# Performance work log

Hardware: AMD Instinct MI355X
Metric: run time of the kernel (lower is better)

## Reference

```python
import jax, jax.numpy as jnp
import numpy as np
from jax import lax

# dims
B, H, W, C = 32, 64, 64, 256
FEATURES, HEADS, NQ = 256, 8, 2
K, STRIDE, PAD = 3, 2, 1
HD = FEATURES // HEADS  # head dim = 32


def setup_inputs() -> dict:
    key = jax.random.key(0)
    ks = jax.random.split(key, 7)
    x = jax.random.normal(ks[0], (B, H, W, C), jnp.float32)
    # learned shared queries: truncated normal * sqrt(1/head_dim)
    query = jax.random.truncated_normal(ks[1], -2.0, 2.0, (NQ, FEATURES), jnp.float32) * np.float32(np.sqrt(1.0 / HD))
    Wk = jax.random.normal(ks[2], (C, FEATURES), jnp.float32) * np.float32(np.sqrt(1.0 / C))  # lecun
    Wv = jax.random.normal(ks[3], (C, FEATURES), jnp.float32) * np.float32(np.sqrt(1.0 / C))
    rpe_bias = jax.random.truncated_normal(ks[4], -2.0, 2.0, (K * K, NQ * HEADS), jnp.float32) * np.float32(0.02)
    attn_scale_w = jax.random.normal(ks[5], (K * K, NQ * HEADS), jnp.float32) * np.float32(0.02)
    Wo = jax.random.normal(ks[6], (FEATURES, FEATURES), jnp.float32) * np.float32(np.sqrt(1.0 / FEATURES))
    return {"x": x, "query": query, "Wk": Wk, "Wv": Wv,
            "rpe_bias": rpe_bias, "attn_scale_w": attn_scale_w, "Wo": Wo}


def _qna_forward(x, query, Wk, Wv, rpe_bias, attn_scale_w, Wo):
    # --- queries: reshape to [NQ, HEADS, HD], unit-normalize per head, depth-scale ---
    q = query.reshape(NQ, HEADS, HD)
    q = q / (jnp.linalg.norm(q, axis=-1, keepdims=True) + 1e-6)
    q = q / jnp.sqrt(HD).astype(q.dtype)

    # --- fused QK: (q Wk^T) applied to x, never materializing per-window keys ---
    Wk_r = Wk.reshape(C, HEADS, HD)
    qWk = jnp.einsum('qHd,DHd->DqH', q, Wk_r)              # [C, NQ, HEADS]
    cost = jnp.einsum('bijD,DqH->bijqH', x, qWk)            # [B, H, W, NQ, HEADS]
    cost_exp = jnp.exp(cost - lax.stop_gradient(jnp.max(cost)))  # global shift, cancels in softmax

    # --- values ---
    v = jnp.einsum('bijD,DF->bijF', x, Wv)                  # [B, H, W, FEATURES]
    v_cost_exp = cost_exp[..., None] * v.reshape(B, H, W, 1, HEADS, HD)
    v_cost_exp = v_cost_exp.reshape(B, H, W, NQ * FEATURES)

    # --- relative position bias + per-offset query mixing scale ---
    rpe = rpe_bias.reshape(K, K, 1, NQ * HEADS)
    rpe_exp = jnp.exp(rpe - lax.stop_gradient(jnp.max(rpe)))  # shift cancels (appears in num & den)
    scale = attn_scale_w.reshape(K, K, 1, NQ * HEADS)
    num_kernel = jnp.repeat(rpe_exp * scale, HD, axis=-1)   # [K, K, 1, NQ*FEATURES]

    # numerator: windowed sum of exp(cost)*v weighted by exp(rpe)*scale (depthwise conv)
    num = lax.conv_general_dilated(
        v_cost_exp, num_kernel, window_strides=(STRIDE, STRIDE),
        padding=((PAD, PAD), (PAD, PAD)), feature_group_count=NQ * FEATURES,
        dimension_numbers=('NHWC', 'HWIO', 'NHWC'))
    # denominator: windowed sum of exp(cost) weighted by exp(rpe)
    den = lax.conv_general_dilated(
        cost_exp.reshape(B, H, W, NQ * HEADS), rpe_exp, window_strides=(STRIDE, STRIDE),
        padding=((PAD, PAD), (PAD, PAD)), feature_group_count=NQ * HEADS,
        dimension_numbers=('NHWC', 'HWIO', 'NHWC'))
    ho, wo = num.shape[1], num.shape[2]

    out = num.reshape(B, ho, wo, NQ, HEADS, HD) / den.reshape(B, ho, wo, NQ, HEADS, 1)
    out = out.sum(axis=3).reshape(B, ho, wo, FEATURES)      # combine queries
    return jnp.einsum('bijF,FO->bijO', out, Wo)             # output projection


def reference(x, query, Wk, Wv, rpe_bias, attn_scale_w, Wo):
    return _qna_forward(x, query, Wk, Wv, rpe_bias, attn_scale_w, Wo)
```

## Files before the change

kernel.cpp:

```cpp
#include <hip/hip_runtime.h>
#include <math.h>

typedef __attribute__((ext_vector_type(8))) short bf16x8;
typedef __attribute__((ext_vector_type(4))) float floatx4;

static __device__ __forceinline__ short f2bf(float f) {
    union { float f; unsigned u; } a; a.f = f;
    unsigned r = a.u + 0x7fffu + ((a.u >> 16) & 1u);
    return (short)(r >> 16);
}
static __device__ __forceinline__ float bf2f(short s) {
    union { unsigned u; float f; } c; c.u = ((unsigned)(unsigned short)s) << 16;
    return c.f;
}

__global__ __launch_bounds__(256) void prep_kernel(
    const float* __restrict__ query,
    const float* __restrict__ Wk,
    const float* __restrict__ rpe_bias,
    const float* __restrict__ attn_scale_w,
    const float* __restrict__ Wv,
    const float* __restrict__ Wo,
    float* __restrict__ rpe_exp,
    float* __restrict__ rpe_scale,
    short* __restrict__ Bq,
    short* __restrict__ Wvh,
    short* __restrict__ Bo)
{
    __shared__ float qn[16 * 33];
    __shared__ float Wt[16][260];
    __shared__ float qwk_s[16][17];
    int tid = threadIdx.x, bb = blockIdx.x;

    for (int i = tid; i < 512; i += 256) {
        int qq  = i >> 8;
        int rem = i & 255;
        int h   = rem >> 5;
        int d   = rem & 31;
        qn[((qq << 3) + h) * 33 + d] = query[i];
    }
    for (int i = tid; i < 16 * 256; i += 256)
        Wt[i >> 8][i & 255] = Wk[bb * 16 * 256 + i];
    __syncthreads();
    if (tid < 16) {
        float s = 0.f;
        #pragma unroll
        for (int d = 0; d < 32; ++d) { float t = qn[tid * 33 + d]; s += t * t; }
        float inv = 1.0f / ((sqrtf(s) + 1e-6f) * sqrtf(32.0f));
        #pragma unroll
        for (int d = 0; d < 32; ++d) qn[tid * 33 + d] *= inv;
    }
    __syncthreads();

    int g  = tid & 15;
    int Dl = tid >> 4;
    int h2 = g & 7;
    float acc = 0.f;
    #pragma unroll
    for (int d = 0; d < 32; ++d)
        acc += qn[g * 33 + d] * Wt[Dl][h2 * 32 + d];
    qwk_s[Dl][g] = acc;
    __syncthreads();

    {
        int kl = tid >> 4, gg = tid & 15;
        int k  = bb * 16 + kl;
        int kc = k >> 5, q5 = k & 31, qd = q5 >> 3, j = q5 & 7;
        int lane = qd * 16 + gg;
        Bq[kc * 512 + lane * 8 + j] = f2bf(qwk_s[kl][gg]);
    }

    for (int kl = 0; kl < 16; ++kl) {
        int k  = bb * 16 + kl;
        int kc = k >> 5, q5 = k & 31, qd = q5 >> 3, j = q5 & 7;
        int n  = tid;
        int gg = n & 15;
        int lane = qd * 16 + gg;
        float vv = Wv[k * 256 + n];
        float vo = Wo[k * 256 + n];
        int nt  = n >> 4;
        Wvh[nt * 4096 + kc * 512 + lane * 8 + j] = f2bf(vv);
        Bo[nt * 4096 + kc * 512 + lane * 8 + j]  = f2bf(vo);
    }

    if (bb == 0 && tid < 144) {
        float r = expf(rpe_bias[tid]);
        rpe_exp[tid]   = r;
        rpe_scale[tid] = r * attn_scale_w[tid];
    }
}

#define XROWA 264
__global__ __launch_bounds__(256) void va_kernel(
    const float* __restrict__ x,
    const short* __restrict__ Bq,
    const short* __restrict__ Wvh,
    short* __restrict__ V,
    float* __restrict__ cesg)
{
    __shared__ short XA[64 * XROWA];
    int tid  = threadIdx.x;
    int lane = tid & 63, wv = tid >> 6;
    int m16  = lane & 15, quad = lane >> 4;
    size_t p0 = (size_t)blockIdx.x * 64;

    #pragma unroll
    for (int i = 0; i < 8; ++i) {
        int it  = tid + i * 256;
        int row = it >> 5, l = it & 31;
        const float* xp = x + (p0 + row) * 256 + l * 8;
        float4 f0 = *(const float4*)xp;
        float4 f1 = *(const float4*)(xp + 4);
        bf16x8 s;
        s[0] = f2bf(f0.x); s[1] = f2bf(f0.y); s[2] = f2bf(f0.z); s[3] = f2bf(f0.w);
        s[4] = f2bf(f1.x); s[5] = f2bf(f1.y); s[6] = f2bf(f1.z); s[7] = f2bf(f1.w);
        *(bf16x8*)&XA[row * XROWA + l * 8] = s;
    }
    __syncthreads();

    bf16x8 Arow[8];
    const short* xrow = &XA[(wv * 16 + m16) * XROWA + quad * 8];
    #pragma unroll
    for (int kc = 0; kc < 8; ++kc)
        Arow[kc] = *(const bf16x8*)(xrow + kc * 32);
    __syncthreads();

    {
        floatx4 acc = (floatx4){0.f, 0.f, 0.f, 0.f};
        const short* bq = Bq + lane * 8;
        #pragma unroll
        for (int kc = 0; kc < 8; ++kc)
            acc = __builtin_amdgcn_mfma_f32_16x16x32_bf16(
                      Arow[kc], *(const bf16x8*)(bq + kc * 512), acc, 0, 0, 0);
        #pragma unroll
        for (int r = 0; r < 4; ++r)
            cesg[(p0 + wv * 16 + quad * 4 + r) * 16 + m16] = expf(acc[r]);
    }

    #pragma unroll 4
    for (int nt = 0; nt < 16; ++nt) {
        floatx4 acc = (floatx4){0.f, 0.f, 0.f, 0.f};
        const short* bp = Wvh + nt * 4096 + lane * 8;
        #pragma unroll
        for (int kc = 0; kc < 8; ++kc)
            acc = __builtin_amdgcn_mfma_f32_16x16x32_bf16(
                      Arow[kc], *(const bf16x8*)(bp + kc * 512), acc, 0, 0, 0);
        #pragma unroll
        for (int r = 0; r < 4; ++r)
            XA[(wv * 16 + quad * 4 + r) * XROWA + nt * 16 + m16] = f2bf(acc[r]);
    }
    __syncthreads();

    #pragma unroll
    for (int i = 0; i < 8; ++i) {
        int it  = tid + i * 256;
        int row = it >> 5, l = it & 31;
        *(bf16x8*)&V[(p0 + row) * 256 + l * 8] =
            *(const bf16x8*)&XA[row * XROWA + l * 8];
    }
}

#define OROW 264
__global__ __launch_bounds__(512) void qb_kernel(
    const float* __restrict__ cesg,
    const short* __restrict__ V,
    const float* __restrict__ rpe_exp,
    const float* __restrict__ rpe_scale,
    const short* __restrict__ Bo,
    float* __restrict__ out)
{
    __shared__ short out_tr[16 * OROW];
    __shared__ float wcoefs[8][9][16];
    __shared__ float invden[16][16];

    int tid  = threadIdx.x;
    int lane = tid & 63, wv = tid >> 6;
    int m16  = lane & 15, quad = lane >> 4;

    int blk0 = blockIdx.x;
    int blk  = ((blk0 & 7) << 8) | (blk0 >> 3);
    int b   = blk >> 6;
    int io  = (blk >> 1) & 31;
    int hf  = blk & 1;
    int i0  = io * 2 - 1;
    int jbase = hf * 32 - 1;

    if (tid < 256) {
        int op = tid >> 4, g = tid & 15;
        float den = 0.f;
        #pragma unroll
        for (int w = 0; w < 9; ++w) {
            int ky = w / 3, kx = w - ky * 3;
            int ii = i0 + ky, jj = jbase + 2 * op + kx;
            if ((unsigned)ii < 64u && (unsigned)jj < 64u) {
                size_t pix = ((size_t)((b << 6) + ii) << 6) + jj;
                den = fmaf(rpe_exp[w * 16 + g], cesg[pix * 16 + g], den);
            }
        }
        invden[op][g] = 1.0f / den;
    }
    __syncthreads();

    for (int it = tid; it < 1152; it += 512) {
        int op = it / 72, r = it - op * 72;
        int w = r >> 3, h = r & 7;
        int ky = w / 3, kx = w - ky * 3;
        int ii = i0 + ky, jj = jbase + 2 * op + kx;
        float v = 0.f;
        if ((unsigned)ii < 64u && (unsigned)jj < 64u) {
            size_t pix = ((size_t)((b << 6) + ii) << 6) + jj;
            v = cesg[pix * 16 + h]     * rpe_scale[w * 16 + h]     * invden[op][h] +
                cesg[pix * 16 + 8 + h] * rpe_scale[w * 16 + 8 + h] * invden[op][8 + h];
        }
        wcoefs[h][w][op] = v;
    }
    __syncthreads();

    {
        int op = tid >> 5;
        int nc = tid & 31;
        int h  = nc >> 2;
        float wcv[9];
        #pragma unroll
        for (int w = 0; w < 9; ++w) wcv[w] = wcoefs[h][w][op];

        float o[8];
        #pragma unroll
        for (int j = 0; j < 8; ++j) o[j] = 0.f;
        #pragma unroll
        for (int w = 0; w < 9; ++w) {
            int ky = w / 3, kx = w - ky * 3;
            int ii = i0 + ky, jj = jbase + 2 * op + kx;
            bool valid = ((unsigned)ii < 64u) && ((unsigned)jj < 64u);
            size_t pix = valid ? (((size_t)((b << 6) + ii) << 6) + jj) : 0;
            bf16x8 vv = *(const bf16x8*)&V[pix * 256 + nc * 8];
            #pragma unroll
            for (int j = 0; j < 8; ++j)
                o[j] = fmaf(wcv[w], bf2f(vv[j]), o[j]);
        }
        bf16x8 ob;
        #pragma unroll
        for (int j = 0; j < 8; ++j) ob[j] = f2bf(o[j]);
        *(bf16x8*)&out_tr[op * OROW + nc * 8] = ob;
    }
    __syncthreads();

    {
        floatx4 acc0 = (floatx4){0.f, 0.f, 0.f, 0.f};
        floatx4 acc1 = (floatx4){0.f, 0.f, 0.f, 0.f};
        int nt0 = wv * 2;
        const short* bp = Bo + nt0 * 4096 + lane * 8;
        #pragma unroll
        for (int kc = 0; kc < 8; ++kc) {
            bf16x8 a  = *(const bf16x8*)&out_tr[m16 * OROW + kc * 32 + quad * 8];
            bf16x8 b0 = *(const bf16x8*)(bp + kc * 512);
            bf16x8 b1 = *(const bf16x8*)(bp + 4096 + kc * 512);
            acc0 = __builtin_amdgcn_mfma_f32_16x16x32_bf16(a, b0, acc0, 0, 0, 0);
            acc1 = __builtin_amdgcn_mfma_f32_16x16x32_bf16(a, b1, acc1, 0, 0, 0);
        }
        size_t op0 = (size_t)blk * 16;
        #pragma unroll
        for (int r = 0; r < 4; ++r) {
            out[(op0 + quad * 4 + r) * 256 + nt0 * 16 + m16]       = acc0[r];
            out[(op0 + quad * 4 + r) * 256 + (nt0 + 1) * 16 + m16] = acc1[r];
        }
    }
}

extern "C" void kernel_launch(void* const* d_in, const int* in_sizes, int n_in,
                              void* d_out, int out_size, void* d_ws, size_t ws_size,
                              hipStream_t stream)
{
    const float* x     = (const float*)d_in[0];
    const float* query = (const float*)d_in[1];
    const float* Wk    = (const float*)d_in[2];
    const float* Wv    = (const float*)d_in[3];
    const float* rpe   = (const float*)d_in[4];
    const float* asw   = (const float*)d_in[5];
    const float* Wo    = (const float*)d_in[6];
    float* out = (float*)d_out;

    float* ws        = (float*)d_ws;
    float* rpe_exp   = ws;
    float* rpe_scale = ws + 144;
    short* Bq        = (short*)(ws + 288);
    short* Wvh       = (short*)(ws + 288 + 2048);
    short* Bo        = (short*)(ws + 288 + 2048 + 32768);
    short* V         = (short*)(ws + 68608);
    float* cesg      = ws + 68608 + 16777216;

    prep_kernel<<<dim3(16), dim3(256), 0, stream>>>(query, Wk, rpe, asw, Wv, Wo,
                                                    rpe_exp, rpe_scale, Bq, Wvh, Bo);
    va_kernel<<<dim3(2048), dim3(256), 0, stream>>>(x, Bq, Wvh, V, cesg);
    qb_kernel<<<dim3(2048), dim3(512), 0, stream>>>(cesg, V, rpe_exp, rpe_scale,
                                                    Bo, out);
}
```

Measured before the change: 289.2 us.

## Retile V projection so each wave owns an N-slice across all rows

```diff
diff --git a/kernel.cpp b/kernel.cpp
--- a/kernel.cpp
+++ b/kernel.cpp
@@ -91,7 +91,7 @@
 }
 
 #define XROWA 264
-__global__ __launch_bounds__(256) void va_kernel(
+__global__ __launch_bounds__(256, 4) void va_kernel(
     const float* __restrict__ x,
     const short* __restrict__ Bq,
     const short* __restrict__ Wvh,
@@ -118,37 +118,54 @@
     }
     __syncthreads();
 
-    bf16x8 Arow[8];
-    const short* xrow = &XA[(wv * 16 + m16) * XROWA + quad * 8];
-    #pragma unroll
-    for (int kc = 0; kc < 8; ++kc)
-        Arow[kc] = *(const bf16x8*)(xrow + kc * 32);
-    __syncthreads();
-
     {
         floatx4 acc = (floatx4){0.f, 0.f, 0.f, 0.f};
-        const short* bq = Bq + lane * 8;
-        #pragma unroll
-        for (int kc = 0; kc < 8; ++kc)
+        const short* bq   = Bq + lane * 8;
+        const short* xrow = &XA[(wv * 16 + m16) * XROWA + quad * 8];
+        #pragma unroll
+        for (int kc = 0; kc < 8; ++kc) {
+            bf16x8 a = *(const bf16x8*)(xrow + kc * 32);
             acc = __builtin_amdgcn_mfma_f32_16x16x32_bf16(
-                      Arow[kc], *(const bf16x8*)(bq + kc * 512), acc, 0, 0, 0);
+                      a, *(const bf16x8*)(bq + kc * 512), acc, 0, 0, 0);
+        }
         #pragma unroll
         for (int r = 0; r < 4; ++r)
             cesg[(p0 + wv * 16 + quad * 4 + r) * 16 + m16] = expf(acc[r]);
     }
 
-    #pragma unroll 4
-    for (int nt = 0; nt < 16; ++nt) {
-        floatx4 acc = (floatx4){0.f, 0.f, 0.f, 0.f};
-        const short* bp = Wvh + nt * 4096 + lane * 8;
-        #pragma unroll
-        for (int kc = 0; kc < 8; ++kc)
-            acc = __builtin_amdgcn_mfma_f32_16x16x32_bf16(
-                      Arow[kc], *(const bf16x8*)(bp + kc * 512), acc, 0, 0, 0);
-        #pragma unroll
-        for (int r = 0; r < 4; ++r)
-            XA[(wv * 16 + quad * 4 + r) * XROWA + nt * 16 + m16] = f2bf(acc[r]);
-    }
+    floatx4 acc[4][4];
+    #pragma unroll
+    for (int m = 0; m < 4; ++m)
+        #pragma unroll
+        for (int ln = 0; ln < 4; ++ln)
+            acc[m][ln] = (floatx4){0.f, 0.f, 0.f, 0.f};
+
+    const short* bvw = Wvh + (4 * wv) * 4096 + lane * 8;
+    #pragma unroll
+    for (int kc = 0; kc < 8; ++kc) {
+        bf16x8 B0 = *(const bf16x8*)(bvw + 0 * 4096 + kc * 512);
+        bf16x8 B1 = *(const bf16x8*)(bvw + 1 * 4096 + kc * 512);
+        bf16x8 B2 = *(const bf16x8*)(bvw + 2 * 4096 + kc * 512);
+        bf16x8 B3 = *(const bf16x8*)(bvw + 3 * 4096 + kc * 512);
+        #pragma unroll
+        for (int m = 0; m < 4; ++m) {
+            bf16x8 a = *(const bf16x8*)&XA[(m * 16 + m16) * XROWA + kc * 32 + quad * 8];
+            acc[m][0] = __builtin_amdgcn_mfma_f32_16x16x32_bf16(a, B0, acc[m][0], 0, 0, 0);
+            acc[m][1] = __builtin_amdgcn_mfma_f32_16x16x32_bf16(a, B1, acc[m][1], 0, 0, 0);
+            acc[m][2] = __builtin_amdgcn_mfma_f32_16x16x32_bf16(a, B2, acc[m][2], 0, 0, 0);
+            acc[m][3] = __builtin_amdgcn_mfma_f32_16x16x32_bf16(a, B3, acc[m][3], 0, 0, 0);
+        }
+    }
+    __syncthreads();
+
+    #pragma unroll
+    for (int m = 0; m < 4; ++m)
+        #pragma unroll
+        for (int ln = 0; ln < 4; ++ln)
+            #pragma unroll
+            for (int r = 0; r < 4; ++r)
+                XA[(m * 16 + quad * 4 + r) * XROWA + (4 * wv + ln) * 16 + m16] =
+                    f2bf(acc[m][ln][r]);
     __syncthreads();
 
     #pragma unroll
```

After: 272.0 us. 1.06x faster.
